# Kernel optimization log

Measured on AMD Instinct MI355X. Metric: run time of the kernel, lower is better.

Reference implementation:

```python
import jax, jax.numpy as jnp
import numpy as np

N_NODES = 100000
N_EDGES = 1600000
B = 256
H = 512
HEADS = 8
DH = H // HEADS


def setup_inputs() -> dict:
    key = jax.random.key(0)
    ks = list(jax.random.split(key, 24))
    def nrm(i, shape, s=0.02):
        return jax.random.normal(ks[i], shape, jnp.float32) * s
    inp = {}
    inp["text_features"] = jax.random.normal(ks[0], (B, 768), jnp.float32)
    inp["video_features"] = jax.random.normal(ks[1], (B, 512), jnp.float32)
    inp["x"] = jax.random.normal(ks[2], (N_NODES, 64), jnp.float32)
    inp["edge_index"] = jax.random.randint(ks[3], (2, N_EDGES), 0, N_NODES, dtype=jnp.int32)
    # sorted node->graph assignment covering all B graphs (no empty segments)
    inp["batch_idx"] = ((jnp.arange(N_NODES) * B) // N_NODES).astype(jnp.int32)
    inp["Wt"] = nrm(4, (768, H)); inp["bt"] = jnp.zeros((H,), jnp.float32)
    inp["Wv"] = nrm(5, (512, H)); inp["bv"] = jnp.zeros((H,), jnp.float32)
    inp["Wq"] = nrm(6, (H, H)); inp["bq"] = jnp.zeros((H,), jnp.float32)
    inp["Wk"] = nrm(7, (H, H)); inp["bk"] = jnp.zeros((H,), jnp.float32)
    inp["Wva"] = nrm(8, (H, H)); inp["bva"] = jnp.zeros((H,), jnp.float32)
    inp["Wo"] = nrm(9, (H, H)); inp["bo"] = jnp.zeros((H,), jnp.float32)
    inp["Wf"] = nrm(10, (2 * H, H)); inp["bf"] = jnp.zeros((H,), jnp.float32)
    inp["G1W"] = nrm(11, (64, 128)); inp["G1b"] = jnp.zeros((128,), jnp.float32)
    inp["G2W"] = nrm(12, (128, 128)); inp["G2b"] = jnp.zeros((128,), jnp.float32)
    inp["G3W"] = nrm(13, (128, 256)); inp["G3b"] = jnp.zeros((256,), jnp.float32)
    inp["Wff"] = nrm(14, (H + 256, H)); inp["bff"] = jnp.zeros((H,), jnp.float32)
    inp["Wb"] = nrm(15, (H, 2)); inp["bb"] = jnp.zeros((2,), jnp.float32)
    inp["Wa"] = nrm(16, (H, 2)); inp["ba"] = jnp.zeros((2,), jnp.float32)
    return inp


def _gcn_conv(h, W, b, src, dst, dis):
    # PyG GCNConv: linear transform, symmetric-normalized aggregation w/ self-loops, bias
    hw = h @ W                                       # [N, C]
    norm = dis[src] * dis[dst]                       # [E]
    msg = hw[src] * norm[:, None]                    # [E, C]
    agg = jax.ops.segment_sum(msg, dst, num_segments=h.shape[0])
    agg = agg + hw * (dis * dis)[:, None]            # self-loop messages
    return agg + b


def reference(text_features, video_features, x, edge_index, batch_idx, Wt, bt, Wv, bv, Wq, bq, Wk, bk, Wva, bva, Wo, bo, Wf, bf, G1W, G1b, G2W, G2b, G3W, G3b, Wff, bff, Wb, bb, Wa, ba):
    # encoders (dropout is eval-mode no-op)
    text_enc = jax.nn.relu(text_features @ Wt + bt)      # [B, H]
    video_enc = jax.nn.relu(video_features @ Wv + bv)    # [B, H]
    # multihead attention; torch seq lens are both 1 (batch acts as N)
    q = (text_enc @ Wq + bq).reshape(B, HEADS, 1, DH)
    k = (video_enc @ Wk + bk).reshape(B, HEADS, 1, DH)
    v = (video_enc @ Wva + bva).reshape(B, HEADS, 1, DH)
    scores = jnp.einsum('bhqd,bhkd->bhqk', q, k) / np.float32(np.sqrt(DH))
    w = jax.nn.softmax(scores, axis=-1)
    attn = jnp.einsum('bhqk,bhkd->bhqd', w, v).reshape(B, H)
    text_attended = attn @ Wo + bo
    # multimodal fusion
    fused = jax.nn.relu(jnp.concatenate([text_attended, video_enc], axis=1) @ Wf + bf)
    # GCN stack
    src, dst = edge_index[0], edge_index[1]
    deg = jax.ops.segment_sum(jnp.ones((N_EDGES,), jnp.float32), dst, num_segments=N_NODES) + 1.0
    dis = jax.lax.rsqrt(deg)
    h = jax.nn.elu(_gcn_conv(x, G1W, G1b, src, dst, dis))
    h = jax.nn.elu(_gcn_conv(h, G2W, G2b, src, dst, dis))
    h = _gcn_conv(h, G3W, G3b, src, dst, dis)            # [N, 256]
    # per-graph mean pooling (the original per-batch Python loop, as one segment-mean)
    counts = jax.ops.segment_sum(jnp.ones((N_NODES,), jnp.float32), batch_idx, num_segments=B)
    pooled = jax.ops.segment_sum(h, batch_idx, num_segments=B) / counts[:, None]  # [B, 256]
    # final fusion + classifier heads
    final = jax.nn.relu(jnp.concatenate([fused, pooled], axis=1) @ Wff + bff)
    bullying = jax.nn.log_softmax(final @ Wb + bb, axis=1)
    aggression = jax.nn.log_softmax(final @ Wa + ba, axis=1)
    return bullying, aggression
```

## Files before the change

kernel.cpp:

```cpp
#include <hip/hip_runtime.h>
#include <hip/hip_bf16.h>
#include <hip/hip_fp8.h>

#define N_NODES 100000
#define NPAD    100096
#define N_EDGES 1600000
#define BATCH   256
#define HDIM    512

typedef unsigned short u16;
typedef unsigned char  u8;
typedef __attribute__((ext_vector_type(8))) short bf16x8;
typedef __attribute__((ext_vector_type(8))) unsigned short u16x8;
typedef __attribute__((ext_vector_type(8))) unsigned char u8x8;
typedef __attribute__((ext_vector_type(4))) float f32x4;

__device__ __forceinline__ float bf2f(u16 u) {
    union { unsigned i; float f; } v; v.i = ((unsigned)u) << 16; return v.f;
}
__device__ __forceinline__ u16 f2bf(float f) {
    __hip_bfloat16 h = __float2bfloat16(f);
    return *reinterpret_cast<u16*>(&h);
}
__device__ __forceinline__ u8 f2fp8(float f) {
    __hip_fp8_e4m3 q(f); return (u8)q.__x;
}
__device__ __forceinline__ float fp82f(u8 b) {
    __hip_fp8_e4m3 q; q.__x = (__hip_fp8_storage_t)b; return (float)q;
}

template<int K, int ACT, int SCALE, int F8>
__global__ __launch_bounds__(256) void gemm_mfma(
        const u16* __restrict__ A, const u16* __restrict__ Wt,
        const float* __restrict__ bias, const float* __restrict__ dis,
        void* __restrict__ Cv, int N) {
    constexpr int RB = K * 2;
    __shared__ u16 As[128 * K];
    __shared__ u16 Bs[128 * K];
    const int tid  = threadIdx.x;
    const int lane = tid & 63;
    const int w    = tid >> 6;
    const int wr   = w >> 1, wc = w & 1;
    const int row0 = blockIdx.y * 128;
    const int col0 = blockIdx.x * 128;

    constexpr int WB     = 128 * RB / 4;
    constexpr int PASSES = WB / 1024;
    const size_t Abase = (size_t)row0 * K;
    const size_t Bbase = (size_t)col0 * K;
    #pragma unroll
    for (int p = 0; p < PASSES; ++p) {
        int Lb  = w * WB + p * 1024;
        int L   = Lb + lane * 16;
        int row = L / RB;
        int cb  = L % RB;
        int scb = cb ^ ((row & 7) << 4);
        const u16* ga = A  + Abase + (size_t)row * K + (scb >> 1);
        const u16* gb = Wt + Bbase + (size_t)row * K + (scb >> 1);
        __builtin_amdgcn_global_load_lds((const __attribute__((address_space(1))) void*)ga,
            (__attribute__((address_space(3))) void*)&As[Lb >> 1], 16, 0, 0);
        __builtin_amdgcn_global_load_lds((const __attribute__((address_space(1))) void*)gb,
            (__attribute__((address_space(3))) void*)&Bs[Lb >> 1], 16, 0, 0);
    }
    asm volatile("s_waitcnt vmcnt(0)" ::: "memory");
    __syncthreads();

    const int rl = lane & 15;
    const int kg = lane >> 4;
    f32x4 acc[4][4] = {};
    #pragma unroll
    for (int s = 0; s < K / 32; ++s) {
        bf16x8 af[4], bg[4];
        #pragma unroll
        for (int m = 0; m < 4; ++m) {
            int row = wr * 64 + m * 16 + rl;
            int cb  = s * 64 + kg * 16;
            int scb = cb ^ ((row & 7) << 4);
            af[m] = *(const bf16x8*)&As[(row * RB + scb) >> 1];
        }
        #pragma unroll
        for (int n = 0; n < 4; ++n) {
            int row = wc * 64 + n * 16 + rl;
            int cb  = s * 64 + kg * 16;
            int scb = cb ^ ((row & 7) << 4);
            bg[n] = *(const bf16x8*)&Bs[(row * RB + scb) >> 1];
        }
        #pragma unroll
        for (int m = 0; m < 4; ++m)
            #pragma unroll
            for (int n = 0; n < 4; ++n)
                acc[m][n] = __builtin_amdgcn_mfma_f32_16x16x32_bf16(af[m], bg[n], acc[m][n], 0, 0, 0);
    }

    #pragma unroll
    for (int m = 0; m < 4; ++m) {
        #pragma unroll
        for (int r = 0; r < 4; ++r) {
            int grow = row0 + wr * 64 + m * 16 + kg * 4 + r;
            float ds = SCALE ? dis[grow] : 1.f;
            #pragma unroll
            for (int n = 0; n < 4; ++n) {
                int gcol = col0 + wc * 64 + n * 16 + rl;
                float v = acc[m][n][r] + bias[gcol];
                if (ACT == 2) v = v > 0.f ? v : expm1f(v);
                v *= ds;
                if (F8) ((u8*)Cv)[(size_t)grow * N + gcol] = f2fp8(v);
                else    ((u16*)Cv)[(size_t)grow * N + gcol] = f2bf(v);
            }
        }
    }
}

template<int ACT>
__global__ __launch_bounds__(256) void gemm64(
        const u16* __restrict__ A, const u16* __restrict__ Wt,
        const float* __restrict__ bias, u16* __restrict__ C,
        int K, int lda, int ldc) {
    __shared__ u16 As[64 * 64];
    __shared__ u16 Bs[64 * 64];
    const int tid  = threadIdx.x;
    const int lane = tid & 63;
    const int w    = tid >> 6;
    const int wr   = w >> 1, wc = w & 1;
    const int row0 = blockIdx.y * 64;
    const int col0 = blockIdx.x * 64;
    const int rl = lane & 15;
    const int kg = lane >> 4;
    f32x4 acc[2][2] = {};

    for (int k0 = 0; k0 < K; k0 += 64) {
        #pragma unroll
        for (int p = 0; p < 2; ++p) {
            int Lb  = w * 2048 + p * 1024;
            int L   = Lb + lane * 16;
            int row = L >> 7;
            int cb  = L & 127;
            int scb = cb ^ ((row & 7) << 4);
            const u16* ga = A  + (size_t)(row0 + row) * lda + k0 + (scb >> 1);
            const u16* gb = Wt + (size_t)(col0 + row) * K   + k0 + (scb >> 1);
            __builtin_amdgcn_global_load_lds((const __attribute__((address_space(1))) void*)ga,
                (__attribute__((address_space(3))) void*)&As[Lb >> 1], 16, 0, 0);
            __builtin_amdgcn_global_load_lds((const __attribute__((address_space(1))) void*)gb,
                (__attribute__((address_space(3))) void*)&Bs[Lb >> 1], 16, 0, 0);
        }
        asm volatile("s_waitcnt vmcnt(0)" ::: "memory");
        __syncthreads();
        #pragma unroll
        for (int s = 0; s < 2; ++s) {
            bf16x8 af[2], bg[2];
            #pragma unroll
            for (int m = 0; m < 2; ++m) {
                int row = wr * 32 + m * 16 + rl;
                int cb  = s * 64 + kg * 16;
                int scb = cb ^ ((row & 7) << 4);
                af[m] = *(const bf16x8*)&As[(row * 128 + scb) >> 1];
            }
            #pragma unroll
            for (int n = 0; n < 2; ++n) {
                int row = wc * 32 + n * 16 + rl;
                int cb  = s * 64 + kg * 16;
                int scb = cb ^ ((row & 7) << 4);
                bg[n] = *(const bf16x8*)&Bs[(row * 128 + scb) >> 1];
            }
            #pragma unroll
            for (int m = 0; m < 2; ++m)
                #pragma unroll
                for (int n = 0; n < 2; ++n)
                    acc[m][n] = __builtin_amdgcn_mfma_f32_16x16x32_bf16(af[m], bg[n], acc[m][n], 0, 0, 0);
        }
        __syncthreads();
    }

    #pragma unroll
    for (int m = 0; m < 2; ++m) {
        #pragma unroll
        for (int r = 0; r < 4; ++r) {
            int grow = row0 + wr * 32 + m * 16 + kg * 4 + r;
            #pragma unroll
            for (int n = 0; n < 2; ++n) {
                int gcol = col0 + wc * 32 + n * 16 + rl;
                float v = acc[m][n][r] + bias[gcol];
                if (ACT == 1) v = fmaxf(v, 0.f);
                C[(size_t)grow * ldc + gcol] = f2bf(v);
            }
        }
    }
}

template<int K, int N>
__device__ __forceinline__ void tw(const float* __restrict__ W, u16* __restrict__ Wt, int t) {
    int n = t / K, k = t - n * K;
    Wt[t] = f2bf(W[(size_t)k * N + n]);
}

#define DEG_BLKS 6250

__global__ void prep_deg(const int* __restrict__ dstE, int* __restrict__ deg,
                         int* __restrict__ slot,
                         const float* __restrict__ G1W, u16* __restrict__ g1wt,
                         const float* __restrict__ G2W, u16* __restrict__ g2wt,
                         const float* __restrict__ Wv,  u16* __restrict__ WvT,
                         const float* __restrict__ Wva, u16* __restrict__ WvaT,
                         const float* __restrict__ Wo,  u16* __restrict__ WoT,
                         const float* __restrict__ Wf,  u16* __restrict__ WfT,
                         const float* __restrict__ video, u16* __restrict__ vidbf) {
    int bid = blockIdx.x;
    const int tid = threadIdx.x;
    if (bid < DEG_BLKS) {
        int e = bid * 256 + tid;
        slot[e] = atomicAdd(&deg[dstE[e]], 1);
        return;
    }
    bid -= DEG_BLKS;
    if (bid < 32)        { tw<64, 128>  (G1W, g1wt, bid * 256 + tid); }
    else if (bid < 96)   { tw<128, 128> (G2W, g2wt, (bid - 32) * 256 + tid); }
    else if (bid < 1120) { tw<512, 512> (Wv,  WvT,  (bid - 96) * 256 + tid); }
    else if (bid < 2144) { tw<512, 512> (Wva, WvaT, (bid - 1120) * 256 + tid); }
    else if (bid < 3168) { tw<512, 512> (Wo,  WoT,  (bid - 2144) * 256 + tid); }
    else if (bid < 5216) { tw<1024, 512>(Wf,  WfT,  (bid - 3168) * 256 + tid); }
    else { int t = (bid - 5216) * 256 + tid; vidbf[t] = f2bf(video[t]); }
}

__global__ void final_fused(const u16* __restrict__ fusedb,
                            const float* __restrict__ pooled, const float* __restrict__ counts,
                            const float* __restrict__ G3W, const float* __restrict__ G3b,
                            const float* __restrict__ Wff, const float* __restrict__ bff,
                            const float* __restrict__ Wb,  const float* __restrict__ bb,
                            const float* __restrict__ Wa,  const float* __restrict__ ba,
                            float* __restrict__ out) {
    __shared__ float cat[768], fin[512], pp[128];
    __shared__ float rd[4][4];
    const int b = blockIdx.x, tid = threadIdx.x;
    cat[tid] = bf2f(fusedb[b * 512 + tid]);
    cat[tid + 256] = bf2f(fusedb[b * 512 + 256 + tid]);
    float inv = 1.f / counts[b];
    if (tid < 128) pp[tid] = pooled[b * 128 + tid] * inv;
    __syncthreads();
    {
        float s = G3b[tid];
        #pragma unroll 8
        for (int k = 0; k < 128; ++k) s += pp[k] * G3W[k * 256 + tid];
        cat[512 + tid] = s;
    }
    __syncthreads();
    {
        float a0 = bff[tid], a1 = bff[tid + 256];
        #pragma unroll 8
        for (int k = 0; k < 768; ++k) {
            float xv = cat[k];
            a0 += xv * Wff[k * 512 + tid];
            a1 += xv * Wff[k * 512 + tid + 256];
        }
        fin[tid] = fmaxf(a0, 0.f);
        fin[tid + 256] = fmaxf(a1, 0.f);
    }
    __syncthreads();
    float z0 = 0.f, z1 = 0.f, y0 = 0.f, y1 = 0.f;
    for (int k = tid; k < 512; k += 256) {
        float f = fin[k];
        z0 += f * Wb[2 * k];
        z1 += f * Wb[2 * k + 1];
        y0 += f * Wa[2 * k];
        y1 += f * Wa[2 * k + 1];
    }
    #pragma unroll
    for (int off = 32; off > 0; off >>= 1) {
        z0 += __shfl_down(z0, off);
        z1 += __shfl_down(z1, off);
        y0 += __shfl_down(y0, off);
        y1 += __shfl_down(y1, off);
    }
    int ww = tid >> 6;
    if ((tid & 63) == 0) { rd[ww][0] = z0; rd[ww][1] = z1; rd[ww][2] = y0; rd[ww][3] = y1; }
    __syncthreads();
    if (tid == 0) {
        float Z0 = rd[0][0] + rd[1][0] + rd[2][0] + rd[3][0] + bb[0];
        float Z1 = rd[0][1] + rd[1][1] + rd[2][1] + rd[3][1] + bb[1];
        float Y0 = rd[0][2] + rd[1][2] + rd[2][2] + rd[3][2] + ba[0];
        float Y1 = rd[0][3] + rd[1][3] + rd[2][3] + rd[3][3] + ba[1];
        float m = fmaxf(Z0, Z1);
        float l = m + logf(expf(Z0 - m) + expf(Z1 - m));
        out[b * 2 + 0] = Z0 - l;
        out[b * 2 + 1] = Z1 - l;
        float m2 = fmaxf(Y0, Y1);
        float l2 = m2 + logf(expf(Y0 - m2) + expf(Y1 - m2));
        out[512 + b * 2 + 0] = Y0 - l2;
        out[512 + b * 2 + 1] = Y1 - l2;
    }
}

__global__ void scan1(const int* __restrict__ in, int* __restrict__ out,
                      int* __restrict__ bsum, float* __restrict__ dis, int n) {
    __shared__ int ts[256];
    const int tid = threadIdx.x;
    const int base = blockIdx.x * 1024;
    int v[4];
    #pragma unroll
    for (int i = 0; i < 4; ++i) {
        int idx = base + tid * 4 + i;
        v[i] = (idx < n) ? in[idx] : 0;
        if (idx < NPAD) dis[idx] = rsqrtf((float)v[i] + 1.f);
    }
    ts[tid] = v[0] + v[1] + v[2] + v[3];
    __syncthreads();
    for (int off = 1; off < 256; off <<= 1) {
        int val = (tid >= off) ? ts[tid - off] : 0;
        __syncthreads();
        ts[tid] += val;
        __syncthreads();
    }
    int run = (tid == 0) ? 0 : ts[tid - 1];
    if (tid == 255) bsum[blockIdx.x] = ts[255];
    #pragma unroll
    for (int i = 0; i < 4; ++i) {
        int idx = base + tid * 4 + i;
        if (idx < n) out[idx] = run;
        run += v[i];
    }
}

__global__ void scan2(int* __restrict__ bsum, int nb) {
    int l = threadIdx.x;
    int a = (l < nb) ? bsum[l] : 0;
    int b = (l + 64 < nb) ? bsum[l + 64] : 0;
    int oa = a, ob = b;
    #pragma unroll
    for (int off = 1; off < 64; off <<= 1) {
        int t = __shfl_up(a, off);
        if (l >= off) a += t;
    }
    int totA = __shfl(a, 63);
    #pragma unroll
    for (int off = 1; off < 64; off <<= 1) {
        int t = __shfl_up(b, off);
        if (l >= off) b += t;
    }
    if (l < nb) bsum[l] = a - oa;
    if (l + 64 < nb) bsum[l + 64] = totA + b - ob;
}

#define SCAT_BLKS 6250
#define SCALE_BLKS 25000
__global__ void scatter_scale(const int* __restrict__ srcE, const int* __restrict__ dstE,
                              const int* __restrict__ partial, const int* __restrict__ bsum,
                              const int* __restrict__ slot,
                              int* __restrict__ csr_src, int* __restrict__ rowptr,
                              const float* __restrict__ x, const float* __restrict__ dis,
                              u16* __restrict__ hs0) {
    const int bid = blockIdx.x, tid = threadIdx.x;
    if (bid < SCAT_BLKS) {
        int e = bid * 256 + tid;
        if (e <= N_NODES) rowptr[e] = (e < N_NODES) ? (partial[e] + bsum[e >> 10]) : N_EDGES;
        int d = dstE[e];
        csr_src[partial[d] + bsum[d >> 10] + slot[e]] = srcE[e];
        return;
    }
    int t = (bid - SCAT_BLKS) * 256 + tid;
    hs0[t] = f2bf(x[t] * dis[t >> 6]);
}

__global__ void csr_agg64(const u16* __restrict__ Hs, const int* __restrict__ rowptr,
                          const int* __restrict__ csr_src, const float* __restrict__ dis,
                          u16* __restrict__ out) {
    int node = blockIdx.x * 4 + (threadIdx.x >> 6);
    if (node >= N_NODES) return;
    int lane = threadIdx.x & 63;
    int g  = lane >> 3;
    int cl = lane & 7;
    int s0 = rowptr[node], s1 = rowptr[node + 1];
    float a[8] = {};
    if (g == 0) {
        u16x8 v = *(const u16x8*)&Hs[(size_t)node * 64 + cl * 8];
        #pragma unroll
        for (int j = 0; j < 8; ++j) a[j] = bf2f(v[j]);
    }
    int e = s0 + g;
    while (e + 24 < s1) {
        int sA = csr_src[e], sB = csr_src[e + 8];
        int sC = csr_src[e + 16], sD = csr_src[e + 24];
        u16x8 vA = *(const u16x8*)&Hs[(size_t)sA * 64 + cl * 8];
        u16x8 vB = *(const u16x8*)&Hs[(size_t)sB * 64 + cl * 8];
        u16x8 vC = *(const u16x8*)&Hs[(size_t)sC * 64 + cl * 8];
        u16x8 vD = *(const u16x8*)&Hs[(size_t)sD * 64 + cl * 8];
        #pragma unroll
        for (int j = 0; j < 8; ++j)
            a[j] += (bf2f(vA[j]) + bf2f(vB[j])) + (bf2f(vC[j]) + bf2f(vD[j]));
        e += 32;
    }
    while (e < s1) {
        int s = csr_src[e];
        u16x8 v = *(const u16x8*)&Hs[(size_t)s * 64 + cl * 8];
        #pragma unroll
        for (int j = 0; j < 8; ++j) a[j] += bf2f(v[j]);
        e += 8;
    }
    #pragma unroll
    for (int m = 8; m < 64; m <<= 1)
        #pragma unroll
        for (int j = 0; j < 8; ++j) a[j] += __shfl_xor(a[j], m);
    if (g == 0) {
        float dd = dis[node];
        u16x8 o;
        #pragma unroll
        for (int j = 0; j < 8; ++j) o[j] = f2bf(a[j] * dd);
        *(u16x8*)&out[(size_t)node * 64 + cl * 8] = o;
    }
}

__global__ void csr_agg_fp8(const u8* __restrict__ Hs, const int* __restrict__ rowptr,
                            const int* __restrict__ csr_src, const float* __restrict__ dis,
                            u16* __restrict__ out) {
    int node = blockIdx.x * 4 + (threadIdx.x >> 6);
    if (node >= N_NODES) return;
    int lane = threadIdx.x & 63;
    int g  = lane >> 4;
    int cl = lane & 15;
    int s0 = rowptr[node], s1 = rowptr[node + 1];
    float a[8] = {};
    if (g == 0) {
        u8x8 v = *(const u8x8*)&Hs[(size_t)node * 128 + cl * 8];
        #pragma unroll
        for (int j = 0; j < 8; ++j) a[j] = fp82f(v[j]);
    }
    int e = s0 + g;
    while (e + 12 < s1) {
        int sA = csr_src[e], sB = csr_src[e + 4];
        int sC = csr_src[e + 8], sD = csr_src[e + 12];
        u8x8 vA = *(const u8x8*)&Hs[(size_t)sA * 128 + cl * 8];
        u8x8 vB = *(const u8x8*)&Hs[(size_t)sB * 128 + cl * 8];
        u8x8 vC = *(const u8x8*)&Hs[(size_t)sC * 128 + cl * 8];
        u8x8 vD = *(const u8x8*)&Hs[(size_t)sD * 128 + cl * 8];
        #pragma unroll
        for (int j = 0; j < 8; ++j)
            a[j] += (fp82f(vA[j]) + fp82f(vB[j])) + (fp82f(vC[j]) + fp82f(vD[j]));
        e += 16;
    }
    while (e < s1) {
        int s = csr_src[e];
        u8x8 v = *(const u8x8*)&Hs[(size_t)s * 128 + cl * 8];
        #pragma unroll
        for (int j = 0; j < 8; ++j) a[j] += fp82f(v[j]);
        e += 4;
    }
    #pragma unroll
    for (int m = 16; m < 64; m <<= 1)
        #pragma unroll
        for (int j = 0; j < 8; ++j) a[j] += __shfl_xor(a[j], m);
    if (g == 0) {
        float dd = dis[node];
        u16x8 o;
        #pragma unroll
        for (int j = 0; j < 8; ++j) o[j] = f2bf(a[j] * dd);
        *(u16x8*)&out[(size_t)node * 128 + cl * 8] = o;
    }
}

__global__ __launch_bounds__(256) void csr_agg_pool(
        const u8* __restrict__ Hs, const int* __restrict__ rowptr,
        const int* __restrict__ csr_src, const float* __restrict__ dis,
        const int* __restrict__ batch,
        float* __restrict__ pooled, float* __restrict__ counts) {
    __shared__ float bins[2][128];
    __shared__ int cnt[2];
    const int tid = threadIdx.x;
    const int base = blockIdx.x * 16;
    if (tid < 128) { bins[0][tid] = 0.f; bins[1][tid] = 0.f; }
    if (tid < 2) cnt[tid] = 0;
    __syncthreads();
    const int lane = tid & 63;
    const int w = tid >> 6;
    const int g = lane >> 4;
    const int cl = lane & 15;
    const int b0 = batch[base];
    #pragma unroll
    for (int i = 0; i < 4; ++i) {
        const int node = base + w * 4 + i;
        const int s0 = rowptr[node], s1 = rowptr[node + 1];
        float a[8] = {};
        if (g == 0) {
            u8x8 v = *(const u8x8*)&Hs[(size_t)node * 128 + cl * 8];
            #pragma unroll
            for (int j = 0; j < 8; ++j) a[j] = fp82f(v[j]);
        }
        int e = s0 + g;
        while (e + 12 < s1) {
            int sA = csr_src[e], sB = csr_src[e + 4];
            int sC = csr_src[e + 8], sD = csr_src[e + 12];
            u8x8 vA = *(const u8x8*)&Hs[(size_t)sA * 128 + cl * 8];
            u8x8 vB = *(const u8x8*)&Hs[(size_t)sB * 128 + cl * 8];
            u8x8 vC = *(const u8x8*)&Hs[(size_t)sC * 128 + cl * 8];
            u8x8 vD = *(const u8x8*)&Hs[(size_t)sD * 128 + cl * 8];
            #pragma unroll
            for (int j = 0; j < 8; ++j)
                a[j] += (fp82f(vA[j]) + fp82f(vB[j])) + (fp82f(vC[j]) + fp82f(vD[j]));
            e += 16;
        }
        while (e < s1) {
            int s = csr_src[e];
            u8x8 v = *(const u8x8*)&Hs[(size_t)s * 128 + cl * 8];
            #pragma unroll
            for (int j = 0; j < 8; ++j) a[j] += fp82f(v[j]);
            e += 4;
        }
        #pragma unroll
        for (int m = 16; m < 64; m <<= 1)
            #pragma unroll
            for (int j = 0; j < 8; ++j) a[j] += __shfl_xor(a[j], m);
        if (g == 0) {
            int bin = (batch[node] != b0) ? 1 : 0;
            float dd = dis[node];
            #pragma unroll
            for (int j = 0; j < 8; ++j) atomicAdd(&bins[bin][cl * 8 + j], a[j] * dd);
            if (cl == 0) atomicAdd(&cnt[bin], 1);
        }
    }
    __syncthreads();
    int bin = tid >> 7, c = tid & 127;
    if (cnt[bin] > 0) atomicAdd(&pooled[(b0 + bin) * 128 + c], bins[bin][c]);
    if (tid < 2 && cnt[tid] > 0) atomicAdd(&counts[b0 + tid], (float)cnt[tid]);
}

extern "C" void kernel_launch(void* const* d_in, const int* in_sizes, int n_in,
                              void* d_out, int out_size, void* d_ws, size_t ws_size,
                              hipStream_t stream) {
    const float* video = (const float*)d_in[1];
    const float* x     = (const float*)d_in[2];
    const int*   eidx  = (const int*)d_in[3];
    const int*   batch = (const int*)d_in[4];
    const float* Wv  = (const float*)d_in[7],  *bv  = (const float*)d_in[8];
    const float* Wva = (const float*)d_in[13], *bva = (const float*)d_in[14];
    const float* Wo  = (const float*)d_in[15], *bo  = (const float*)d_in[16];
    const float* Wf  = (const float*)d_in[17], *bf  = (const float*)d_in[18];
    const float* G1W = (const float*)d_in[19], *G1b = (const float*)d_in[20];
    const float* G2W = (const float*)d_in[21], *G2b = (const float*)d_in[22];
    const float* G3W = (const float*)d_in[23], *G3b = (const float*)d_in[24];
    const float* Wff = (const float*)d_in[25], *bff = (const float*)d_in[26];
    const float* Wb  = (const float*)d_in[27], *bb  = (const float*)d_in[28];
    const float* Wa  = (const float*)d_in[29], *ba  = (const float*)d_in[30];
    const int* srcE = eidx;
    const int* dstE = eidx + N_EDGES;

    char* wsc = (char*)d_ws;
    size_t off = 0;
    auto alloc = [&](size_t bytes) { char* p = wsc + off; off += (bytes + 255) & ~(size_t)255; return p; };
    u16*   bufA    = (u16*)  alloc((size_t)NPAD * 128 * 2);
    u16*   bufB    = (u16*)  alloc((size_t)NPAD * 128 * 2);
    float* dis     = (float*)alloc(NPAD * 4);
    int*   deg     = (int*)  alloc(NPAD * 4);
    float* pooled  = (float*)alloc((BATCH * 128 + BATCH) * 4);
    float* counts  = pooled + BATCH * 128;
    int*   partial = (int*)  alloc(N_NODES * 4);
    int*   rowptr  = (int*)  alloc((N_NODES + 1) * 4);
    int*   slot    = (int*)  alloc((size_t)N_EDGES * 4);
    int*   csrsrc  = (int*)  alloc((size_t)N_EDGES * 4);
    int*   bsum    = (int*)  alloc(128 * 4);
    u16*   g1wt    = (u16*)  alloc(128 * 64 * 2);
    u16*   g2wt    = (u16*)  alloc(128 * 128 * 2);
    u16*   WvT     = (u16*)  alloc(512 * 512 * 2);
    u16*   WvaT    = (u16*)  alloc(512 * 512 * 2);
    u16*   WoT     = (u16*)  alloc(512 * 512 * 2);
    u16*   WfT     = (u16*)  alloc(512 * 1024 * 2);
    u16*   vidbf   = (u16*)  alloc(BATCH * 512 * 2);
    u16*   catb    = (u16*)  alloc(BATCH * 1024 * 2);
    u16*   vattnb  = (u16*)  alloc(BATCH * 512 * 2);
    u16*   fusedb  = (u16*)  alloc(BATCH * 512 * 2);

    const int NB = (N_NODES + 1023) / 1024;

    hipMemsetAsync(deg, 0, NPAD * 4 + (BATCH * 128 + BATCH) * 4, stream);

    prep_deg<<<DEG_BLKS + 5728, 256, 0, stream>>>(dstE, deg, slot,
        G1W, g1wt, G2W, g2wt, Wv, WvT, Wva, WvaT, Wo, WoT, Wf, WfT, video, vidbf);

    scan1<<<NB, 256, 0, stream>>>(deg, partial, bsum, dis, N_NODES);
    scan2<<<1, 64, 0, stream>>>(bsum, NB);
    scatter_scale<<<SCAT_BLKS + SCALE_BLKS, 256, 0, stream>>>(
        srcE, dstE, partial, bsum, slot, csrsrc, rowptr, x, dis, bufA);

    dim3 fe512(8, 4);
    gemm64<1><<<fe512, 256, 0, stream>>>(vidbf, WvT, bv, catb + 512, 512, 512, 1024);
    gemm64<0><<<fe512, 256, 0, stream>>>(catb + 512, WvaT, bva, vattnb, 512, 1024, 512);
    gemm64<0><<<fe512, 256, 0, stream>>>(vattnb, WoT, bo, catb, 512, 512, 1024);
    gemm64<1><<<fe512, 256, 0, stream>>>(catb, WfT, bf, fusedb, 1024, 1024, 512);

    csr_agg64<<<(N_NODES + 3) / 4, 256, 0, stream>>>(bufA, rowptr, csrsrc, dis, bufB);
    gemm_mfma<64, 2, 1, 1><<<dim3(1, NPAD / 128), 256, 0, stream>>>(
        bufB, g1wt, G1b, dis, bufA, 128);
    csr_agg_fp8<<<(N_NODES + 3) / 4, 256, 0, stream>>>((const u8*)bufA, rowptr, csrsrc, dis, bufB);
    gemm_mfma<128, 2, 1, 1><<<dim3(1, NPAD / 128), 256, 0, stream>>>(
        bufB, g2wt, G2b, dis, bufA, 128);
    csr_agg_pool<<<N_NODES / 16, 256, 0, stream>>>((const u8*)bufA, rowptr, csrsrc, dis,
                                                   batch, pooled, counts);

    final_fused<<<BATCH, 256, 0, stream>>>(fusedb, pooled, counts, G3W, G3b,
                                           Wff, bff, Wb, bb, Wa, ba, (float*)d_out);
}
```

Baseline: 434.1 us.

## Store (src,dst) pairs in CSR and pool last layer edge-parallel

The CSR array now stores src and dst pairs, so the final aggregation-plus-pooling step can walk edges in flat chunks of 1024 instead of walking nodes. This removes the per-node degree imbalance, and a separate block range handles the self-loop terms and node counts. Partial sums are flushed per graph segment through shared-memory bins, falling back to global atomics. In exchange the CSR array doubles in size, which adds memory traffic in the scatter and in both earlier aggregation kernels, since those still read only the src field through an 8-byte stride.

```diff
diff --git a/kernel.cpp b/kernel.cpp
--- a/kernel.cpp
+++ b/kernel.cpp
@@ -344,7 +344,7 @@
 __global__ void scatter_scale(const int* __restrict__ srcE, const int* __restrict__ dstE,
                               const int* __restrict__ partial, const int* __restrict__ bsum,
                               const int* __restrict__ slot,
-                              int* __restrict__ csr_src, int* __restrict__ rowptr,
+                              int2* __restrict__ csr_sd, int* __restrict__ rowptr,
                               const float* __restrict__ x, const float* __restrict__ dis,
                               u16* __restrict__ hs0) {
     const int bid = blockIdx.x, tid = threadIdx.x;
@@ -352,7 +352,7 @@
         int e = bid * 256 + tid;
         if (e <= N_NODES) rowptr[e] = (e < N_NODES) ? (partial[e] + bsum[e >> 10]) : N_EDGES;
         int d = dstE[e];
-        csr_src[partial[d] + bsum[d >> 10] + slot[e]] = srcE[e];
+        csr_sd[partial[d] + bsum[d >> 10] + slot[e]] = make_int2(srcE[e], d);
         return;
     }
     int t = (bid - SCAT_BLKS) * 256 + tid;
@@ -360,7 +360,7 @@
 }
 
 __global__ void csr_agg64(const u16* __restrict__ Hs, const int* __restrict__ rowptr,
-                          const int* __restrict__ csr_src, const float* __restrict__ dis,
+                          const int2* __restrict__ csr_sd, const float* __restrict__ dis,
                           u16* __restrict__ out) {
     int node = blockIdx.x * 4 + (threadIdx.x >> 6);
     if (node >= N_NODES) return;
@@ -376,8 +376,8 @@
     }
     int e = s0 + g;
     while (e + 24 < s1) {
-        int sA = csr_src[e], sB = csr_src[e + 8];
-        int sC = csr_src[e + 16], sD = csr_src[e + 24];
+        int sA = csr_sd[e].x, sB = csr_sd[e + 8].x;
+        int sC = csr_sd[e + 16].x, sD = csr_sd[e + 24].x;
         u16x8 vA = *(const u16x8*)&Hs[(size_t)sA * 64 + cl * 8];
         u16x8 vB = *(const u16x8*)&Hs[(size_t)sB * 64 + cl * 8];
         u16x8 vC = *(const u16x8*)&Hs[(size_t)sC * 64 + cl * 8];
@@ -388,7 +388,7 @@
         e += 32;
     }
     while (e < s1) {
-        int s = csr_src[e];
+        int s = csr_sd[e].x;
         u16x8 v = *(const u16x8*)&Hs[(size_t)s * 64 + cl * 8];
         #pragma unroll
         for (int j = 0; j < 8; ++j) a[j] += bf2f(v[j]);
@@ -408,7 +408,7 @@
 }
 
 __global__ void csr_agg_fp8(const u8* __restrict__ Hs, const int* __restrict__ rowptr,
-                            const int* __restrict__ csr_src, const float* __restrict__ dis,
+                            const int2* __restrict__ csr_sd, const float* __restrict__ dis,
                             u16* __restrict__ out) {
     int node = blockIdx.x * 4 + (threadIdx.x >> 6);
     if (node >= N_NODES) return;
@@ -424,8 +424,8 @@
     }
     int e = s0 + g;
     while (e + 12 < s1) {
-        int sA = csr_src[e], sB = csr_src[e + 4];
-        int sC = csr_src[e + 8], sD = csr_src[e + 12];
+        int sA = csr_sd[e].x, sB = csr_sd[e + 4].x;
+        int sC = csr_sd[e + 8].x, sD = csr_sd[e + 12].x;
         u8x8 vA = *(const u8x8*)&Hs[(size_t)sA * 128 + cl * 8];
         u8x8 vB = *(const u8x8*)&Hs[(size_t)sB * 128 + cl * 8];
         u8x8 vC = *(const u8x8*)&Hs[(size_t)sC * 128 + cl * 8];
@@ -436,7 +436,7 @@
         e += 16;
     }
     while (e < s1) {
-        int s = csr_src[e];
+        int s = csr_sd[e].x;
         u8x8 v = *(const u8x8*)&Hs[(size_t)s * 128 + cl * 8];
         #pragma unroll
         for (int j = 0; j < 8; ++j) a[j] += fp82f(v[j]);
@@ -455,69 +455,82 @@
     }
 }
 
-__global__ __launch_bounds__(256) void csr_agg_pool(
-        const u8* __restrict__ Hs, const int* __restrict__ rowptr,
-        const int* __restrict__ csr_src, const float* __restrict__ dis,
-        const int* __restrict__ batch,
+#define PE_BLKS 1563
+#define PS_BLKS 391
+__global__ __launch_bounds__(256) void pool_fused(
+        const u8* __restrict__ Hs, const int2* __restrict__ csr_sd,
+        const float* __restrict__ dis, const int* __restrict__ batch,
         float* __restrict__ pooled, float* __restrict__ counts) {
     __shared__ float bins[2][128];
-    __shared__ int cnt[2];
+    __shared__ int b0s;
     const int tid = threadIdx.x;
-    const int base = blockIdx.x * 16;
+    const int bid = blockIdx.x;
     if (tid < 128) { bins[0][tid] = 0.f; bins[1][tid] = 0.f; }
-    if (tid < 2) cnt[tid] = 0;
-    __syncthreads();
-    const int lane = tid & 63;
-    const int w = tid >> 6;
-    const int g = lane >> 4;
-    const int cl = lane & 15;
-    const int b0 = batch[base];
-    #pragma unroll
-    for (int i = 0; i < 4; ++i) {
-        const int node = base + w * 4 + i;
-        const int s0 = rowptr[node], s1 = rowptr[node + 1];
+    if (bid < PE_BLKS) {
+        const int base = bid * 1024;
+        const int end  = min(base + 1024, N_EDGES);
+        if (tid == 0) b0s = batch[csr_sd[base].y];
+        __syncthreads();
+        const int b0 = b0s;
+        const int lane = tid & 63, w = tid >> 6;
+        const int slot = w * 4 + (lane >> 4);
+        const int cl = lane & 15;
         float a[8] = {};
-        if (g == 0) {
-            u8x8 v = *(const u8x8*)&Hs[(size_t)node * 128 + cl * 8];
-            #pragma unroll
-            for (int j = 0; j < 8; ++j) a[j] = fp82f(v[j]);
-        }
-        int e = s0 + g;
-        while (e + 12 < s1) {
-            int sA = csr_src[e], sB = csr_src[e + 4];
-            int sC = csr_src[e + 8], sD = csr_src[e + 12];
-            u8x8 vA = *(const u8x8*)&Hs[(size_t)sA * 128 + cl * 8];
-            u8x8 vB = *(const u8x8*)&Hs[(size_t)sB * 128 + cl * 8];
-            u8x8 vC = *(const u8x8*)&Hs[(size_t)sC * 128 + cl * 8];
-            u8x8 vD = *(const u8x8*)&Hs[(size_t)sD * 128 + cl * 8];
-            #pragma unroll
-            for (int j = 0; j < 8; ++j)
-                a[j] += (fp82f(vA[j]) + fp82f(vB[j])) + (fp82f(vC[j]) + fp82f(vD[j]));
-            e += 16;
-        }
-        while (e < s1) {
-            int s = csr_src[e];
-            u8x8 v = *(const u8x8*)&Hs[(size_t)s * 128 + cl * 8];
-            #pragma unroll
-            for (int j = 0; j < 8; ++j) a[j] += fp82f(v[j]);
-            e += 4;
-        }
-        #pragma unroll
-        for (int m = 16; m < 64; m <<= 1)
-            #pragma unroll
-            for (int j = 0; j < 8; ++j) a[j] += __shfl_xor(a[j], m);
-        if (g == 0) {
-            int bin = (batch[node] != b0) ? 1 : 0;
-            float dd = dis[node];
-            #pragma unroll
-            for (int j = 0; j < 8; ++j) atomicAdd(&bins[bin][cl * 8 + j], a[j] * dd);
-            if (cl == 0) atomicAdd(&cnt[bin], 1);
-        }
-    }
-    __syncthreads();
-    int bin = tid >> 7, c = tid & 127;
-    if (cnt[bin] > 0) atomicAdd(&pooled[(b0 + bin) * 128 + c], bins[bin][c]);
-    if (tid < 2 && cnt[tid] > 0) atomicAdd(&counts[b0 + tid], (float)cnt[tid]);
+        int bcur = b0;
+        for (int e = base + slot; e < end; e += 16) {
+            int2 sd = csr_sd[e];
+            float dd = dis[sd.y];
+            int b = batch[sd.y];
+            if (b != bcur) {
+                if (bcur - b0 < 2) {
+                    #pragma unroll
+                    for (int j = 0; j < 8; ++j) atomicAdd(&bins[bcur - b0][cl * 8 + j], a[j]);
+                } else {
+                    #pragma unroll
+                    for (int j = 0; j < 8; ++j) atomicAdd(&pooled[bcur * 128 + cl * 8 + j], a[j]);
+                }
+                #pragma unroll
+                for (int j = 0; j < 8; ++j) a[j] = 0.f;
+                bcur = b;
+            }
+            u8x8 v = *(const u8x8*)&Hs[(size_t)sd.x * 128 + cl * 8];
+            #pragma unroll
+            for (int j = 0; j < 8; ++j) a[j] += fp82f(v[j]) * dd;
+        }
+        if (bcur - b0 < 2) {
+            #pragma unroll
+            for (int j = 0; j < 8; ++j) atomicAdd(&bins[bcur - b0][cl * 8 + j], a[j]);
+        } else {
+            #pragma unroll
+            for (int j = 0; j < 8; ++j) atomicAdd(&pooled[bcur * 128 + cl * 8 + j], a[j]);
+        }
+        __syncthreads();
+        int bin = tid >> 7, c = tid & 127;
+        if (b0 + bin < BATCH) atomicAdd(&pooled[(b0 + bin) * 128 + c], bins[bin][c]);
+    } else {
+        const int base = (bid - PE_BLKS) * 256;
+        const int end  = min(base + 256, N_NODES);
+        if (tid == 0) b0s = batch[base];
+        __syncthreads();
+        const int b0 = b0s;
+        const int c = tid & 127, h = tid >> 7;
+        float a = 0.f; int bcur = b0; int cnt = 0;
+        for (int n = base + h; n < end; n += 2) {
+            int b = batch[n];
+            if (b != bcur) {
+                atomicAdd(&bins[bcur - b0][c], a);
+                if (c == 0) atomicAdd(&counts[bcur], (float)cnt);
+                a = 0.f; cnt = 0; bcur = b;
+            }
+            a += fp82f(Hs[(size_t)n * 128 + c]) * dis[n];
+            cnt++;
+        }
+        atomicAdd(&bins[bcur - b0][c], a);
+        if (c == 0) atomicAdd(&counts[bcur], (float)cnt);
+        __syncthreads();
+        int bin = tid >> 7, cc = tid & 127;
+        if (b0 + bin < BATCH) atomicAdd(&pooled[(b0 + bin) * 128 + cc], bins[bin][cc]);
+    }
 }
 
 extern "C" void kernel_launch(void* const* d_in, const int* in_sizes, int n_in,
@@ -552,7 +565,7 @@
     int*   partial = (int*)  alloc(N_NODES * 4);
     int*   rowptr  = (int*)  alloc((N_NODES + 1) * 4);
     int*   slot    = (int*)  alloc((size_t)N_EDGES * 4);
-    int*   csrsrc  = (int*)  alloc((size_t)N_EDGES * 4);
+    int2*  csr_sd  = (int2*) alloc((size_t)N_EDGES * 8);
     int*   bsum    = (int*)  alloc(128 * 4);
     u16*   g1wt    = (u16*)  alloc(128 * 64 * 2);
     u16*   g2wt    = (u16*)  alloc(128 * 128 * 2);
@@ -575,7 +588,7 @@
     scan1<<<NB, 256, 0, stream>>>(deg, partial, bsum, dis, N_NODES);
     scan2<<<1, 64, 0, stream>>>(bsum, NB);
     scatter_scale<<<SCAT_BLKS + SCALE_BLKS, 256, 0, stream>>>(
-        srcE, dstE, partial, bsum, slot, csrsrc, rowptr, x, dis, bufA);
+        srcE, dstE, partial, bsum, slot, csr_sd, rowptr, x, dis, bufA);
 
     dim3 fe512(8, 4);
     gemm64<1><<<fe512, 256, 0, stream>>>(vidbf, WvT, bv, catb + 512, 512, 512, 1024);
@@ -583,14 +596,14 @@
     gemm64<0><<<fe512, 256, 0, stream>>>(vattnb, WoT, bo, catb, 512, 512, 1024);
     gemm64<1><<<fe512, 256, 0, stream>>>(catb, WfT, bf, fusedb, 1024, 1024, 512);
 
-    csr_agg64<<<(N_NODES + 3) / 4, 256, 0, stream>>>(bufA, rowptr, csrsrc, dis, bufB);
+    csr_agg64<<<(N_NODES + 3) / 4, 256, 0, stream>>>(bufA, rowptr, csr_sd, dis, bufB);
     gemm_mfma<64, 2, 1, 1><<<dim3(1, NPAD / 128), 256, 0, stream>>>(
         bufB, g1wt, G1b, dis, bufA, 128);
-    csr_agg_fp8<<<(N_NODES + 3) / 4, 256, 0, stream>>>((const u8*)bufA, rowptr, csrsrc, dis, bufB);
+    csr_agg_fp8<<<(N_NODES + 3) / 4, 256, 0, stream>>>((const u8*)bufA, rowptr, csr_sd, dis, bufB);
     gemm_mfma<128, 2, 1, 1><<<dim3(1, NPAD / 128), 256, 0, stream>>>(
         bufB, g2wt, G2b, dis, bufA, 128);
-    csr_agg_pool<<<N_NODES / 16, 256, 0, stream>>>((const u8*)bufA, rowptr, csrsrc, dis,
-                                                   batch, pooled, counts);
+    pool_fused<<<PE_BLKS + PS_BLKS, 256, 0, stream>>>((const u8*)bufA, csr_sd, dis,
+                                                      batch, pooled, counts);
 
     final_fused<<<BATCH, 256, 0, stream>>>(fusedb, pooled, counts, G3W, G3b,
                                            Wff, bff, Wb, bb, Wa, ba, (float*)d_out);
```

After: 427.5 us. No clear change (-1.5%).
